# Performance work log

Measured on AMD Instinct MI355X. Metric: run time of the kernel, lower is better.

## Reference

```python
import jax, jax.numpy as jnp
import numpy as np

NUM_GROUPS = 32
EPS = 1e-05
HEAD_DIM = 1


def setup_inputs() -> dict:
    key = jax.random.key(0)
    ks = jax.random.split(key, 10)
    B, C, H, W = 2, 128, 32, 32
    s = 1.0 / np.sqrt(C)
    return {
        "hidden_states": jax.random.normal(ks[0], (B, C, H, W), dtype=jnp.float32),
        "gn_weight": jnp.ones((C,), dtype=jnp.float32),
        "gn_bias": jnp.zeros((C,), dtype=jnp.float32),
        "Wq": jax.random.normal(ks[1], (C, C), dtype=jnp.float32) * s,
        "bq": jnp.zeros((C,), dtype=jnp.float32),
        "Wk": jax.random.normal(ks[2], (C, C), dtype=jnp.float32) * s,
        "bk": jnp.zeros((C,), dtype=jnp.float32),
        "Wv": jax.random.normal(ks[3], (C, C), dtype=jnp.float32) * s,
        "bv": jnp.zeros((C,), dtype=jnp.float32),
        "Wo": jax.random.normal(ks[4], (C, C), dtype=jnp.float32) * s,
        "bo": jnp.zeros((C,), dtype=jnp.float32),
    }


def reference(hidden_states, gn_weight, gn_bias, Wq, bq, Wk, bk, Wv, bv, Wo, bo):
    B, C, H, W = hidden_states.shape
    S = H * W
    n_heads = C // HEAD_DIM  # = C since HEAD_DIM=1

    # GroupNorm over (C//G, H, W) within each group
    xg = hidden_states.reshape(B, NUM_GROUPS, C // NUM_GROUPS, S)
    mean = xg.mean(axis=(2, 3), keepdims=True)
    var = xg.var(axis=(2, 3), keepdims=True)
    xn = (xg - mean) * jax.lax.rsqrt(var + EPS)
    xn = xn.reshape(B, C, S) * gn_weight[None, :, None] + gn_bias[None, :, None]

    h = xn.transpose(0, 2, 1)  # [B, S, C]
    q = h @ Wq.T + bq
    k = h @ Wk.T + bk
    v = h @ Wv.T + bv

    # [B, S, C] -> [B, n_heads, S, HEAD_DIM]
    q = q.reshape(B, S, n_heads, HEAD_DIM).transpose(0, 2, 1, 3)
    k = k.reshape(B, S, n_heads, HEAD_DIM).transpose(0, 2, 1, 3)
    v = v.reshape(B, S, n_heads, HEAD_DIM).transpose(0, 2, 1, 3)

    scale = 1.0 / np.sqrt(HEAD_DIM)
    scores = jnp.einsum('bhqd,bhkd->bhqk', q, k) * scale  # [B, n_heads, S, S]
    attn = jax.nn.softmax(scores, axis=-1)
    out = jnp.einsum('bhqk,bhkd->bhqd', attn, v)  # [B, n_heads, S, HEAD_DIM]

    out = out.transpose(0, 2, 1, 3).reshape(B, S, C)
    out = out @ Wo.T + bo
    out = out.transpose(0, 2, 1).reshape(B, C, H, W)
    return out + hidden_states
```

## Files before the change

### kernel.cpp

```cpp
#include <hip/hip_runtime.h>
#include <math.h>

#define S 1024
#define C 128

#if __has_builtin(__builtin_amdgcn_exp2f)
__device__ __forceinline__ float EXP2(float x) { return __builtin_amdgcn_exp2f(x); }
#else
__device__ __forceinline__ float EXP2(float x) {
  float r; asm("v_exp_f32 %0, %1" : "=v"(r) : "v"(x)); return r;
}
#endif

__device__ __forceinline__ float wred_sum(float v) {
  #pragma unroll
  for (int off = 32; off; off >>= 1) v += __shfl_xor(v, off);
  return v;
}

__global__ __launch_bounds__(256) void prep_kernel(const float* __restrict__ x,
                                                   const float* __restrict__ w,
                                                   const float* __restrict__ bias,
                                                   const float* __restrict__ Wq,
                                                   const float* __restrict__ Wk,
                                                   const float* __restrict__ Wv,
                                                   const float* __restrict__ Wo,
                                                   float* __restrict__ xn,
                                                   float* __restrict__ WT) {
  if (blockIdx.x >= 64) {
    int idx = (blockIdx.x - 64) * 256 + threadIdx.x;
    int mat = idx >> 14, n = (idx >> 7) & 127, k = idx & 127;
    const float* W = mat == 0 ? Wq : (mat == 1 ? Wk : (mat == 2 ? Wv : Wo));
    WT[k * 512 + mat * 128 + n] = W[n * 128 + k];
    return;
  }
  const int b = blockIdx.x >> 5, g = blockIdx.x & 31;
  const float* xp = x + (size_t)(b * C + g * 4) * S;
  float* xnp = xn + (size_t)(b * C + g * 4) * S;
  float4 vals[4];
  float s = 0.f, ss = 0.f;
  #pragma unroll
  for (int i = 0; i < 4; ++i) {
    float4 v = ((const float4*)xp)[threadIdx.x + i * 256];
    vals[i] = v;
    s += (v.x + v.y) + (v.z + v.w);
    ss += v.x * v.x; ss += v.y * v.y; ss += v.z * v.z; ss += v.w * v.w;
  }
  s = wred_sum(s); ss = wred_sum(ss);
  __shared__ float red[8];
  const int lane = threadIdx.x & 63, wid = threadIdx.x >> 6;
  if (lane == 0) { red[wid] = s; red[4 + wid] = ss; }
  __syncthreads();
  float ts = (red[0] + red[1]) + (red[2] + red[3]);
  float tss = (red[4] + red[5]) + (red[6] + red[7]);
  float mean = ts * (1.f / 4096.f);
  float var = tss * (1.f / 4096.f) - mean * mean;
  float rstd = rsqrtf(var + 1e-5f);
  #pragma unroll
  for (int i = 0; i < 4; ++i) {
    float sc = w[g * 4 + i] * rstd;
    float sh = fmaf(-mean, sc, bias[g * 4 + i]);
    float4 v = vals[i];
    float4 o = make_float4(fmaf(v.x, sc, sh), fmaf(v.y, sc, sh),
                           fmaf(v.z, sc, sh), fmaf(v.w, sc, sh));
    ((float4*)xnp)[threadIdx.x + i * 256] = o;
  }
}

__global__ __launch_bounds__(256) void gemm_qkv(const float* __restrict__ xn,
                                                const float* __restrict__ WT,
                                                const float* __restrict__ bq,
                                                const float* __restrict__ bk,
                                                const float* __restrict__ bv,
                                                float* __restrict__ qkv) {
  const int m0 = blockIdx.x * 64;
  const int nt = blockIdx.y;
  const int b = blockIdx.z;
  const int mat = nt >> 2, nloc = (nt & 3) * 32;
  const int col0 = mat * 128 + nloc;
  const float* biasp = (mat == 0 ? bq : (mat == 1 ? bk : bv)) + nloc;
  const float* Ab = xn + (size_t)b * C * S + m0;
  float* outp = qkv + ((size_t)mat * 2 + b) * (C * S) + (size_t)nloc * S + m0;

  __shared__ float As[32][64];
  __shared__ float Bs[32][32];
  const int tx = threadIdx.x & 15, ty = threadIdx.x >> 4;
  float acc[2][4] = {};

  for (int kt = 0; kt < 4; ++kt) {
    const int k0 = kt * 32;
    __syncthreads();
    #pragma unroll
    for (int i = threadIdx.x; i < 2048; i += 256) {
      int kk = i >> 6, mm = i & 63;
      As[kk][mm] = Ab[(size_t)(k0 + kk) * S + mm];
    }
    #pragma unroll
    for (int i = threadIdx.x; i < 1024; i += 256) {
      int kk = i >> 5, nn = i & 31;
      Bs[kk][nn] = WT[(k0 + kk) * 512 + col0 + nn];
    }
    __syncthreads();
    #pragma unroll
    for (int kk = 0; kk < 32; ++kk) {
      float4 a4 = *(const float4*)&As[kk][tx * 4];
      float2 b2 = *(const float2*)&Bs[kk][ty * 2];
      float av[4] = {a4.x, a4.y, a4.z, a4.w};
      float bv2[2] = {b2.x, b2.y};
      #pragma unroll
      for (int j = 0; j < 2; ++j)
        #pragma unroll
        for (int i = 0; i < 4; ++i)
          acc[j][i] = fmaf(bv2[j], av[i], acc[j][i]);
    }
  }
  #pragma unroll
  for (int j = 0; j < 2; ++j) {
    float bj = biasp[ty * 2 + j];
    float4 o = make_float4(acc[j][0] + bj, acc[j][1] + bj, acc[j][2] + bj, acc[j][3] + bj);
    *(float4*)&outp[(size_t)(ty * 2 + j) * S + tx * 4] = o;
  }
}

__global__ __launch_bounds__(128) void attn_kernel(const float* __restrict__ qkv,
                                                   float* __restrict__ attnb) {
  const int h = blockIdx.y, b = blockIdx.z;
  const size_t base = ((size_t)b * C + h) * S;
  const float* qp = qkv + base;
  const float* kp = qkv + 2 * C * S + base;
  const float* vp = qkv + 4 * C * S + base;
  __shared__ float kl[S];
  __shared__ float vl[S];
  __shared__ float red[4];
  float kmax = -1e30f, kmin = 1e30f;
  #pragma unroll
  for (int i = threadIdx.x; i < 256; i += 128) {
    float4 k4 = ((const float4*)kp)[i];
    float4 v4 = ((const float4*)vp)[i];
    ((float4*)kl)[i] = k4;
    ((float4*)vl)[i] = v4;
    kmax = fmaxf(kmax, fmaxf(fmaxf(k4.x, k4.y), fmaxf(k4.z, k4.w)));
    kmin = fminf(kmin, fminf(fminf(k4.x, k4.y), fminf(k4.z, k4.w)));
  }
  #pragma unroll
  for (int off = 32; off; off >>= 1) {
    kmax = fmaxf(kmax, __shfl_xor(kmax, off));
    kmin = fminf(kmin, __shfl_xor(kmin, off));
  }
  const int lane = threadIdx.x & 63, wid = threadIdx.x >> 6;
  if (lane == 0) { red[wid] = kmax; red[2 + wid] = kmin; }
  __syncthreads();
  kmax = fmaxf(red[0], red[1]);
  kmin = fminf(red[2], red[3]);

  const int qi = blockIdx.x * 128 + threadIdx.x;
  const float LOG2E = 1.4426950408889634f;
  float qs = qp[qi] * LOG2E;
  float nmb = -fmaxf(qs * kmax, qs * kmin);
  float den0 = 0.f, den1 = 0.f, den2 = 0.f, den3 = 0.f;
  float num0 = 0.f, num1 = 0.f, num2 = 0.f, num3 = 0.f;
  #pragma unroll 4
  for (int j8 = 0; j8 < S / 8; ++j8) {
    float4 ka = ((const float4*)kl)[2 * j8];
    float4 kb = ((const float4*)kl)[2 * j8 + 1];
    float4 va = ((const float4*)vl)[2 * j8];
    float4 vb = ((const float4*)vl)[2 * j8 + 1];
    float e0 = EXP2(fmaf(qs, ka.x, nmb));
    float e1 = EXP2(fmaf(qs, ka.y, nmb));
    float e2 = EXP2(fmaf(qs, ka.z, nmb));
    float e3 = EXP2(fmaf(qs, ka.w, nmb));
    float e4 = EXP2(fmaf(qs, kb.x, nmb));
    float e5 = EXP2(fmaf(qs, kb.y, nmb));
    float e6 = EXP2(fmaf(qs, kb.z, nmb));
    float e7 = EXP2(fmaf(qs, kb.w, nmb));
    den0 += e0; num0 = fmaf(e0, va.x, num0);
    den1 += e1; num1 = fmaf(e1, va.y, num1);
    den2 += e2; num2 = fmaf(e2, va.z, num2);
    den3 += e3; num3 = fmaf(e3, va.w, num3);
    den0 += e4; num0 = fmaf(e4, vb.x, num0);
    den1 += e5; num1 = fmaf(e5, vb.y, num1);
    den2 += e6; num2 = fmaf(e6, vb.z, num2);
    den3 += e7; num3 = fmaf(e7, vb.w, num3);
  }
  float num = (num0 + num1) + (num2 + num3);
  float den = (den0 + den1) + (den2 + den3);
  attnb[base + qi] = num / den;
}

__global__ __launch_bounds__(256) void gemm_out(const float* __restrict__ attnb,
                                                const float* __restrict__ WT,
                                                const float* __restrict__ bo,
                                                const float* __restrict__ x,
                                                float* __restrict__ out) {
  const int m0 = blockIdx.x * 64;
  const int b = blockIdx.z;
  const int nloc = blockIdx.y * 32;
  const int col0 = 384 + nloc;
  const float* Ab = attnb + (size_t)b * C * S + m0;
  const float* biasp = bo + nloc;
  const float* resp = x + (size_t)b * C * S + (size_t)nloc * S + m0;
  float* outp = out + (size_t)b * C * S + (size_t)nloc * S + m0;

  __shared__ float As[32][64];
  __shared__ float Bs[32][32];
  const int tx = threadIdx.x & 15, ty = threadIdx.x >> 4;
  float acc[2][4] = {};

  for (int kt = 0; kt < 4; ++kt) {
    const int k0 = kt * 32;
    __syncthreads();
    #pragma unroll
    for (int i = threadIdx.x; i < 2048; i += 256) {
      int kk = i >> 6, mm = i & 63;
      As[kk][mm] = Ab[(size_t)(k0 + kk) * S + mm];
    }
    #pragma unroll
    for (int i = threadIdx.x; i < 1024; i += 256) {
      int kk = i >> 5, nn = i & 31;
      Bs[kk][nn] = WT[(k0 + kk) * 512 + col0 + nn];
    }
    __syncthreads();
    #pragma unroll
    for (int kk = 0; kk < 32; ++kk) {
      float4 a4 = *(const float4*)&As[kk][tx * 4];
      float2 b2 = *(const float2*)&Bs[kk][ty * 2];
      float av[4] = {a4.x, a4.y, a4.z, a4.w};
      float bv2[2] = {b2.x, b2.y};
      #pragma unroll
      for (int j = 0; j < 2; ++j)
        #pragma unroll
        for (int i = 0; i < 4; ++i)
          acc[j][i] = fmaf(bv2[j], av[i], acc[j][i]);
    }
  }
  #pragma unroll
  for (int j = 0; j < 2; ++j) {
    float bj = biasp[ty * 2 + j];
    const float* rrow = resp + (size_t)(ty * 2 + j) * S + tx * 4;
    float4 r = *(const float4*)rrow;
    float4 o = make_float4(acc[j][0] + bj + r.x, acc[j][1] + bj + r.y,
                           acc[j][2] + bj + r.z, acc[j][3] + bj + r.w);
    *(float4*)&outp[(size_t)(ty * 2 + j) * S + tx * 4] = o;
  }
}

extern "C" void kernel_launch(void* const* d_in, const int* in_sizes, int n_in,
                              void* d_out, int out_size, void* d_ws, size_t ws_size,
                              hipStream_t stream) {
  const float* x  = (const float*)d_in[0];
  const float* gw = (const float*)d_in[1];
  const float* gb = (const float*)d_in[2];
  const float* Wq = (const float*)d_in[3];
  const float* bq = (const float*)d_in[4];
  const float* Wk = (const float*)d_in[5];
  const float* bk = (const float*)d_in[6];
  const float* Wv = (const float*)d_in[7];
  const float* bv = (const float*)d_in[8];
  const float* Wo = (const float*)d_in[9];
  const float* bo = (const float*)d_in[10];
  float* out = (float*)d_out;

  float* ws = (float*)d_ws;
  float* xn  = ws;
  float* qkv = ws + 262144;
  float* WT  = ws + 262144 + 786432;

  hipLaunchKernelGGL(prep_kernel, dim3(320), dim3(256), 0, stream,
                     x, gw, gb, Wq, Wk, Wv, Wo, xn, WT);
  hipLaunchKernelGGL(gemm_qkv, dim3(16, 12, 2), dim3(256), 0, stream, xn, WT, bq, bk, bv, qkv);
  hipLaunchKernelGGL(attn_kernel, dim3(8, 128, 2), dim3(128), 0, stream, qkv, xn);
  hipLaunchKernelGGL(gemm_out, dim3(16, 4, 2), dim3(256), 0, stream, xn, WT, bo, x, out);
}
```

Measured before the change: 140.2 us.

## Pack attention math into float2 vectors, two queries per thread; retile GEMMs with full-K staging

```diff
diff --git a/kernel.cpp b/kernel.cpp
--- a/kernel.cpp
+++ b/kernel.cpp
@@ -11,6 +11,8 @@
   float r; asm("v_exp_f32 %0, %1" : "=v"(r) : "v"(x)); return r;
 }
 #endif
+
+typedef float v2f __attribute__((ext_vector_type(2)));
 
 __device__ __forceinline__ float wred_sum(float v) {
   #pragma unroll
@@ -82,37 +84,36 @@
   const float* Ab = xn + (size_t)b * C * S + m0;
   float* outp = qkv + ((size_t)mat * 2 + b) * (C * S) + (size_t)nloc * S + m0;
 
-  __shared__ float As[32][64];
-  __shared__ float Bs[32][32];
+  __shared__ float As[128][64];
+  __shared__ float Bs[128][32];
   const int tx = threadIdx.x & 15, ty = threadIdx.x >> 4;
+
+  #pragma unroll
+  for (int t = 0; t < 8; ++t) {
+    int i = threadIdx.x + t * 256;
+    int kk = i >> 4, m4 = (i & 15) * 4;
+    *(float4*)&As[kk][m4] = *(const float4*)&Ab[(size_t)kk * S + m4];
+  }
+  #pragma unroll
+  for (int t = 0; t < 4; ++t) {
+    int i = threadIdx.x + t * 256;
+    int kk = i >> 3, n4 = (i & 7) * 4;
+    *(float4*)&Bs[kk][n4] = *(const float4*)&WT[kk * 512 + col0 + n4];
+  }
+  __syncthreads();
+
   float acc[2][4] = {};
-
-  for (int kt = 0; kt < 4; ++kt) {
-    const int k0 = kt * 32;
-    __syncthreads();
+  #pragma unroll 8
+  for (int kk = 0; kk < 128; ++kk) {
+    float4 a4 = *(const float4*)&As[kk][tx * 4];
+    float2 b2 = *(const float2*)&Bs[kk][ty * 2];
+    float av[4] = {a4.x, a4.y, a4.z, a4.w};
+    float bv2[2] = {b2.x, b2.y};
     #pragma unroll
-    for (int i = threadIdx.x; i < 2048; i += 256) {
-      int kk = i >> 6, mm = i & 63;
-      As[kk][mm] = Ab[(size_t)(k0 + kk) * S + mm];
-    }
-    #pragma unroll
-    for (int i = threadIdx.x; i < 1024; i += 256) {
-      int kk = i >> 5, nn = i & 31;
-      Bs[kk][nn] = WT[(k0 + kk) * 512 + col0 + nn];
-    }
-    __syncthreads();
-    #pragma unroll
-    for (int kk = 0; kk < 32; ++kk) {
-      float4 a4 = *(const float4*)&As[kk][tx * 4];
-      float2 b2 = *(const float2*)&Bs[kk][ty * 2];
-      float av[4] = {a4.x, a4.y, a4.z, a4.w};
-      float bv2[2] = {b2.x, b2.y};
+    for (int j = 0; j < 2; ++j)
       #pragma unroll
-      for (int j = 0; j < 2; ++j)
-        #pragma unroll
-        for (int i = 0; i < 4; ++i)
-          acc[j][i] = fmaf(bv2[j], av[i], acc[j][i]);
-    }
+      for (int i = 0; i < 4; ++i)
+        acc[j][i] = fmaf(bv2[j], av[i], acc[j][i]);
   }
   #pragma unroll
   for (int j = 0; j < 2; ++j) {
@@ -153,38 +154,49 @@
   kmax = fmaxf(red[0], red[1]);
   kmin = fminf(red[2], red[3]);
 
-  const int qi = blockIdx.x * 128 + threadIdx.x;
   const float LOG2E = 1.4426950408889634f;
-  float qs = qp[qi] * LOG2E;
-  float nmb = -fmaxf(qs * kmax, qs * kmin);
-  float den0 = 0.f, den1 = 0.f, den2 = 0.f, den3 = 0.f;
-  float num0 = 0.f, num1 = 0.f, num2 = 0.f, num3 = 0.f;
-  #pragma unroll 4
+  const int qi = blockIdx.x * 256 + threadIdx.x;
+  float qsA = qp[qi] * LOG2E;
+  float qsB = qp[qi + 128] * LOG2E;
+  float nmA = -fmaxf(qsA * kmax, qsA * kmin);
+  float nmB = -fmaxf(qsB * kmax, qsB * kmin);
+  v2f qA = {qsA, qsA}, qB = {qsB, qsB};
+  v2f nA = {nmA, nmA}, nB = {nmB, nmB};
+  v2f dA0 = {0.f, 0.f}, dA1 = {0.f, 0.f}, uA0 = {0.f, 0.f}, uA1 = {0.f, 0.f};
+  v2f dB0 = {0.f, 0.f}, dB1 = {0.f, 0.f}, uB0 = {0.f, 0.f}, uB1 = {0.f, 0.f};
+
+  #pragma unroll 2
   for (int j8 = 0; j8 < S / 8; ++j8) {
     float4 ka = ((const float4*)kl)[2 * j8];
     float4 kb = ((const float4*)kl)[2 * j8 + 1];
     float4 va = ((const float4*)vl)[2 * j8];
     float4 vb = ((const float4*)vl)[2 * j8 + 1];
-    float e0 = EXP2(fmaf(qs, ka.x, nmb));
-    float e1 = EXP2(fmaf(qs, ka.y, nmb));
-    float e2 = EXP2(fmaf(qs, ka.z, nmb));
-    float e3 = EXP2(fmaf(qs, ka.w, nmb));
-    float e4 = EXP2(fmaf(qs, kb.x, nmb));
-    float e5 = EXP2(fmaf(qs, kb.y, nmb));
-    float e6 = EXP2(fmaf(qs, kb.z, nmb));
-    float e7 = EXP2(fmaf(qs, kb.w, nmb));
-    den0 += e0; num0 = fmaf(e0, va.x, num0);
-    den1 += e1; num1 = fmaf(e1, va.y, num1);
-    den2 += e2; num2 = fmaf(e2, va.z, num2);
-    den3 += e3; num3 = fmaf(e3, va.w, num3);
-    den0 += e4; num0 = fmaf(e4, vb.x, num0);
-    den1 += e5; num1 = fmaf(e5, vb.y, num1);
-    den2 += e6; num2 = fmaf(e6, vb.z, num2);
-    den3 += e7; num3 = fmaf(e7, vb.w, num3);
-  }
-  float num = (num0 + num1) + (num2 + num3);
-  float den = (den0 + den1) + (den2 + den3);
-  attnb[base + qi] = num / den;
+    v2f k01 = {ka.x, ka.y}, k23 = {ka.z, ka.w}, k45 = {kb.x, kb.y}, k67 = {kb.z, kb.w};
+    v2f v01 = {va.x, va.y}, v23 = {va.z, va.w}, v45 = {vb.x, vb.y}, v67 = {vb.z, vb.w};
+    v2f a, e;
+    a = qA * k01 + nA; e.x = EXP2(a.x); e.y = EXP2(a.y);
+    dA0 += e; uA0 += e * v01;
+    a = qA * k23 + nA; e.x = EXP2(a.x); e.y = EXP2(a.y);
+    dA1 += e; uA1 += e * v23;
+    a = qA * k45 + nA; e.x = EXP2(a.x); e.y = EXP2(a.y);
+    dA0 += e; uA0 += e * v45;
+    a = qA * k67 + nA; e.x = EXP2(a.x); e.y = EXP2(a.y);
+    dA1 += e; uA1 += e * v67;
+    a = qB * k01 + nB; e.x = EXP2(a.x); e.y = EXP2(a.y);
+    dB0 += e; uB0 += e * v01;
+    a = qB * k23 + nB; e.x = EXP2(a.x); e.y = EXP2(a.y);
+    dB1 += e; uB1 += e * v23;
+    a = qB * k45 + nB; e.x = EXP2(a.x); e.y = EXP2(a.y);
+    dB0 += e; uB0 += e * v45;
+    a = qB * k67 + nB; e.x = EXP2(a.x); e.y = EXP2(a.y);
+    dB1 += e; uB1 += e * v67;
+  }
+  float numA = (uA0.x + uA0.y) + (uA1.x + uA1.y);
+  float denA = (dA0.x + dA0.y) + (dA1.x + dA1.y);
+  float numB = (uB0.x + uB0.y) + (uB1.x + uB1.y);
+  float denB = (dB0.x + dB0.y) + (dB1.x + dB1.y);
+  attnb[base + qi] = numA / denA;
+  attnb[base + qi + 128] = numB / denB;
 }
 
 __global__ __launch_bounds__(256) void gemm_out(const float* __restrict__ attnb,
@@ -192,56 +204,47 @@
                                                 const float* __restrict__ bo,
                                                 const float* __restrict__ x,
                                                 float* __restrict__ out) {
-  const int m0 = blockIdx.x * 64;
+  const int m0 = blockIdx.x * 32;
   const int b = blockIdx.z;
   const int nloc = blockIdx.y * 32;
   const int col0 = 384 + nloc;
   const float* Ab = attnb + (size_t)b * C * S + m0;
-  const float* biasp = bo + nloc;
+  float* outp = out + (size_t)b * C * S + (size_t)nloc * S + m0;
   const float* resp = x + (size_t)b * C * S + (size_t)nloc * S + m0;
-  float* outp = out + (size_t)b * C * S + (size_t)nloc * S + m0;
-
-  __shared__ float As[32][64];
-  __shared__ float Bs[32][32];
-  const int tx = threadIdx.x & 15, ty = threadIdx.x >> 4;
-  float acc[2][4] = {};
-
-  for (int kt = 0; kt < 4; ++kt) {
-    const int k0 = kt * 32;
-    __syncthreads();
-    #pragma unroll
-    for (int i = threadIdx.x; i < 2048; i += 256) {
-      int kk = i >> 6, mm = i & 63;
-      As[kk][mm] = Ab[(size_t)(k0 + kk) * S + mm];
-    }
-    #pragma unroll
-    for (int i = threadIdx.x; i < 1024; i += 256) {
-      int kk = i >> 5, nn = i & 31;
-      Bs[kk][nn] = WT[(k0 + kk) * 512 + col0 + nn];
-    }
-    __syncthreads();
-    #pragma unroll
-    for (int kk = 0; kk < 32; ++kk) {
-      float4 a4 = *(const float4*)&As[kk][tx * 4];
-      float2 b2 = *(const float2*)&Bs[kk][ty * 2];
-      float av[4] = {a4.x, a4.y, a4.z, a4.w};
-      float bv2[2] = {b2.x, b2.y};
-      #pragma unroll
-      for (int j = 0; j < 2; ++j)
-        #pragma unroll
-        for (int i = 0; i < 4; ++i)
-          acc[j][i] = fmaf(bv2[j], av[i], acc[j][i]);
-    }
-  }
-  #pragma unroll
-  for (int j = 0; j < 2; ++j) {
-    float bj = biasp[ty * 2 + j];
-    const float* rrow = resp + (size_t)(ty * 2 + j) * S + tx * 4;
-    float4 r = *(const float4*)rrow;
-    float4 o = make_float4(acc[j][0] + bj + r.x, acc[j][1] + bj + r.y,
-                           acc[j][2] + bj + r.z, acc[j][3] + bj + r.w);
-    *(float4*)&outp[(size_t)(ty * 2 + j) * S + tx * 4] = o;
-  }
+
+  __shared__ float As[128][32];
+  __shared__ float Bs[128][32];
+  const int tx = threadIdx.x & 7, ty = threadIdx.x >> 3;
+
+  #pragma unroll
+  for (int t = 0; t < 4; ++t) {
+    int i = threadIdx.x + t * 256;
+    int kk = i >> 3, m4 = (i & 7) * 4;
+    *(float4*)&As[kk][m4] = *(const float4*)&Ab[(size_t)kk * S + m4];
+  }
+  #pragma unroll
+  for (int t = 0; t < 4; ++t) {
+    int i = threadIdx.x + t * 256;
+    int kk = i >> 3, n4 = (i & 7) * 4;
+    *(float4*)&Bs[kk][n4] = *(const float4*)&WT[kk * 512 + col0 + n4];
+  }
+  __syncthreads();
+
+  float acc[4] = {};
+  #pragma unroll 8
+  for (int kk = 0; kk < 128; ++kk) {
+    float4 a4 = *(const float4*)&As[kk][tx * 4];
+    float bb = Bs[kk][ty];
+    acc[0] = fmaf(bb, a4.x, acc[0]);
+    acc[1] = fmaf(bb, a4.y, acc[1]);
+    acc[2] = fmaf(bb, a4.z, acc[2]);
+    acc[3] = fmaf(bb, a4.w, acc[3]);
+  }
+  float bj = bo[nloc + ty];
+  const float4 r = *(const float4*)&resp[(size_t)ty * S + tx * 4];
+  float4 o = make_float4(acc[0] + bj + r.x, acc[1] + bj + r.y,
+                         acc[2] + bj + r.z, acc[3] + bj + r.w);
+  *(float4*)&outp[(size_t)ty * S + tx * 4] = o;
 }
 
 extern "C" void kernel_launch(void* const* d_in, const int* in_sizes, int n_in,
@@ -268,6 +271,6 @@
   hipLaunchKernelGGL(prep_kernel, dim3(320), dim3(256), 0, stream,
                      x, gw, gb, Wq, Wk, Wv, Wo, xn, WT);
   hipLaunchKernelGGL(gemm_qkv, dim3(16, 12, 2), dim3(256), 0, stream, xn, WT, bq, bk, bv, qkv);
-  hipLaunchKernelGGL(attn_kernel, dim3(8, 128, 2), dim3(128), 0, stream, qkv, xn);
-  hipLaunchKernelGGL(gemm_out, dim3(16, 4, 2), dim3(256), 0, stream, xn, WT, bo, x, out);
-}
+  hipLaunchKernelGGL(attn_kernel, dim3(4, 128, 2), dim3(128), 0, stream, qkv, xn);
+  hipLaunchKernelGGL(gemm_out, dim3(32, 4, 2), dim3(256), 0, stream, xn, WT, bo, x, out);
+}
```

New measurement: 120.7 us. -13.9%, faster.
